# Kernel optimization log

Hardware: AMD Instinct MI355X
Metric: run time of the kernel (lower is better)

Reference implementation:

```python
import jax, jax.numpy as jnp
import numpy as np

B, K, D = 4, 4096, 2048

def setup_inputs() -> dict:
    key = jax.random.key(0)
    k1, k2, k3 = jax.random.split(key, 3)
    x = jax.random.normal(k1, (B, K, D), dtype=jnp.float32)
    # Conv1d(dim, dim, kernel_size=1) weight [D, D, 1] squeezed to a dense [D_out, D_in] matrix
    W = jax.random.normal(k2, (D, D), dtype=jnp.float32) / np.sqrt(D)
    b = jax.random.normal(k3, (D,), dtype=jnp.float32) * 0.02
    return {"x": x, "W": W, "b": b}

def reference(x, W, b):
    # lam_t = sigmoid(dt_proj(u_t)); pointwise conv1d == per-timestep linear
    lam = jax.nn.sigmoid(jnp.einsum("bkd,ed->bke", x, W) + b)  # [B,K,D]
    # Gated linear recurrence: s_t = lam_t * s_{t-1} + (1 - lam_t) * u_t
    def step(s, inp):
        lam_t, u_t = inp  # each [B,D]
        s = lam_t * s + (1.0 - lam_t) * u_t
        return s, s
    s0 = jnp.zeros((x.shape[0], x.shape[2]), dtype=x.dtype)
    _, ys = jax.lax.scan(step, s0, (jnp.moveaxis(lam, 1, 0), jnp.moveaxis(x, 1, 0)))
    return jnp.moveaxis(ys, 0, 1)  # [B,K,D]
```

## Files before the change

### kernel.cpp

```cpp
#include <hip/hip_runtime.h>
#include <hip/hip_bf16.h>

#define B_SZ 4
#define K_SEQ 4096
#define D_DIM 2048
#define M_ROWS (B_SZ * K_SEQ)

#define BM 128
#define BN 128
#define BK 32

#define CHUNK 64
#define NCHUNK (K_SEQ / CHUNK)

typedef __attribute__((ext_vector_type(8))) short short8;
typedef __attribute__((ext_vector_type(4))) float floatx4;
typedef __attribute__((ext_vector_type(8))) unsigned short ushortx8;

__device__ __forceinline__ unsigned short f2bf_rne(float f) {
  unsigned int u = __float_as_uint(f);
  u += 0x7fffu + ((u >> 16) & 1u);
  return (unsigned short)(u >> 16);
}
__device__ __forceinline__ float bf2f(unsigned short u) {
  return __uint_as_float(((unsigned int)u) << 16);
}

#define NX4 (M_ROWS * D_DIM / 4)
#define NW4 (D_DIM * D_DIM / 4)
__global__ void cvt_bf16_kernel(const float* __restrict__ x,
                                const float* __restrict__ W,
                                unsigned short* __restrict__ xb,
                                unsigned short* __restrict__ Wb) {
  int i = blockIdx.x * blockDim.x + threadIdx.x;
  const float* src;
  unsigned short* dst;
  int j;
  if (i < NX4) { src = x; dst = xb; j = i; }
  else         { src = W; dst = Wb; j = i - NX4; }
  float4 v = ((const float4*)src)[j];
  ushort4 o;
  o.x = f2bf_rne(v.x);
  o.y = f2bf_rne(v.y);
  o.z = f2bf_rne(v.z);
  o.w = f2bf_rne(v.w);
  ((ushort4*)dst)[j] = o;
}

__device__ __forceinline__ void gl_lds16(const void* g, void* l) {
  __builtin_amdgcn_global_load_lds(
      (const __attribute__((address_space(1))) unsigned int*)g,
      (__attribute__((address_space(3))) unsigned int*)l, 16, 0, 0);
}

template <bool GBF>
__global__ __launch_bounds__(256)
void gemm_lam_kernel(const unsigned short* __restrict__ A,
                     const unsigned short* __restrict__ Wb,
                     const float* __restrict__ bias,
                     void* __restrict__ lamv) {
  __shared__ __align__(16) unsigned short As[BM * BK];
  __shared__ __align__(16) unsigned short Bs[BN * BK];

  const int tid = threadIdx.x;
  const int lane = tid & 63;
  const int wave = tid >> 6;
  const int bm = blockIdx.x * BM;
  const int bn = blockIdx.y * BN;
  const int wr = (wave >> 1) * 64;
  const int wc = (wave & 1) * 64;
  const int lrow = lane & 15;
  const int kgrp = lane >> 4;

  floatx4 acc[4][4];
#pragma unroll
  for (int i = 0; i < 4; ++i)
#pragma unroll
    for (int j = 0; j < 4; ++j)
      acc[i][j] = (floatx4){0.f, 0.f, 0.f, 0.f};

  const int c0 = tid, c1 = tid + 256;
  const int r0 = c0 >> 2, q0 = (c0 & 3) ^ ((r0 >> 1) & 3);
  const int r1 = c1 >> 2, q1 = (c1 & 3) ^ ((r1 >> 1) & 3);
  const unsigned short* gA0 = A + (size_t)(bm + r0) * D_DIM + (q0 << 3);
  const unsigned short* gA1 = A + (size_t)(bm + r1) * D_DIM + (q1 << 3);
  const unsigned short* gB0 = Wb + (size_t)(bn + r0) * D_DIM + (q0 << 3);
  const unsigned short* gB1 = Wb + (size_t)(bn + r1) * D_DIM + (q1 << 3);
  unsigned short* lA0 = As + c0 * 8;
  unsigned short* lA1 = As + c1 * 8;
  unsigned short* lB0 = Bs + c0 * 8;
  unsigned short* lB1 = Bs + c1 * 8;

  const int kq_s = kgrp ^ ((lrow >> 1) & 3);

  for (int k0 = 0; k0 < D_DIM; k0 += BK) {
    gl_lds16(gA0 + k0, lA0);
    gl_lds16(gA1 + k0, lA1);
    gl_lds16(gB0 + k0, lB0);
    gl_lds16(gB1 + k0, lB1);
    __syncthreads();

    short8 af[4], bf[4];
#pragma unroll
    for (int i = 0; i < 4; ++i) {
      const int rowA = wr + i * 16 + lrow;
      const int rowB = wc + i * 16 + lrow;
      af[i] = *(const short8*)(As + rowA * 32 + kq_s * 8);
      bf[i] = *(const short8*)(Bs + rowB * 32 + kq_s * 8);
    }
#pragma unroll
    for (int mi = 0; mi < 4; ++mi)
#pragma unroll
      for (int ni = 0; ni < 4; ++ni)
        acc[mi][ni] = __builtin_amdgcn_mfma_f32_16x16x32_bf16(
            af[mi], bf[ni], acc[mi][ni], 0, 0, 0);
    __syncthreads();
  }

  const int crow = (lane >> 4) << 2;
  const int ccol = lane & 15;
#pragma unroll
  for (int ni = 0; ni < 4; ++ni) {
    const int ge = bn + wc + ni * 16 + ccol;
    const float bb = bias[ge];
#pragma unroll
    for (int mi = 0; mi < 4; ++mi) {
      const int gm0 = bm + wr + mi * 16 + crow;
#pragma unroll
      for (int r = 0; r < 4; ++r) {
        float v = acc[mi][ni][r] + bb;
        size_t off = (size_t)(gm0 + r) * D_DIM + ge;
        if constexpr (GBF) {
          float g = 1.0f / (1.0f + __expf(v));
          ((unsigned short*)lamv)[off] = f2bf_rne(g);
        } else {
          ((float*)lamv)[off] = 1.0f / (1.0f + __expf(-v));
        }
      }
    }
  }
}


__global__ void scan_reduce_bf(const unsigned short* __restrict__ gb,
                               const unsigned short* __restrict__ xb,
                               float* __restrict__ Ach,
                               float* __restrict__ Bch) {
  int idx = blockIdx.x * blockDim.x + threadIdx.x;
  int d8 = idx & 255;
  int c = (idx >> 8) & (NCHUNK - 1);
  int b = idx >> 14;
  size_t base = ((size_t)(b * K_SEQ + c * CHUNK)) * D_DIM + d8 * 8;
  float A[8], Bv[8];
#pragma unroll
  for (int j = 0; j < 8; ++j) { A[j] = 1.f; Bv[j] = 0.f; }
#pragma unroll 8
  for (int t = 0; t < CHUNK; ++t) {
    size_t o = base + (size_t)t * D_DIM;
    ushortx8 g8 = *(const ushortx8*)(gb + o);
    ushortx8 u8 = *(const ushortx8*)(xb + o);
#pragma unroll
    for (int j = 0; j < 8; ++j) {
      float g = bf2f(g8[j]), u = bf2f(u8[j]);
      A[j] -= g * A[j];
      Bv[j] += g * (u - Bv[j]);
    }
  }
  float4 a0 = make_float4(A[0], A[1], A[2], A[3]);
  float4 a1 = make_float4(A[4], A[5], A[6], A[7]);
  float4 b0 = make_float4(Bv[0], Bv[1], Bv[2], Bv[3]);
  float4 b1 = make_float4(Bv[4], Bv[5], Bv[6], Bv[7]);
  ((float4*)Ach)[idx * 2] = a0;
  ((float4*)Ach)[idx * 2 + 1] = a1;
  ((float4*)Bch)[idx * 2] = b0;
  ((float4*)Bch)[idx * 2 + 1] = b1;
}

__global__ void scan_prefix_kernel(const float* __restrict__ Ach,
                                   const float* __restrict__ Bch,
                                   float* __restrict__ Sst) {
  int idx = blockIdx.x * blockDim.x + threadIdx.x;
  int d4 = idx & (D_DIM / 4 - 1);
  int b = idx >> 9;
  float4 s = make_float4(0.f, 0.f, 0.f, 0.f);
#pragma unroll 4
  for (int c = 0; c < NCHUNK; ++c) {
    int o4 = (b * NCHUNK + c) * (D_DIM / 4) + d4;
    ((float4*)Sst)[o4] = s;
    float4 A = ((const float4*)Ach)[o4];
    float4 Bv = ((const float4*)Bch)[o4];
    s.x = A.x * s.x + Bv.x;
    s.y = A.y * s.y + Bv.y;
    s.z = A.z * s.z + Bv.z;
    s.w = A.w * s.w + Bv.w;
  }
}

__global__ void scan_apply_bf(const unsigned short* __restrict__ gb,
                              const unsigned short* __restrict__ xb,
                              const float* __restrict__ Sst,
                              float* __restrict__ out) {
  int idx = blockIdx.x * blockDim.x + threadIdx.x;
  int d8 = idx & 255;
  int c = (idx >> 8) & (NCHUNK - 1);
  int b = idx >> 14;
  size_t base = ((size_t)(b * K_SEQ + c * CHUNK)) * D_DIM + d8 * 8;
  float4 s0 = ((const float4*)Sst)[idx * 2];
  float4 s1 = ((const float4*)Sst)[idx * 2 + 1];
  float s[8] = {s0.x, s0.y, s0.z, s0.w, s1.x, s1.y, s1.z, s1.w};
#pragma unroll 8
  for (int t = 0; t < CHUNK; ++t) {
    size_t o = base + (size_t)t * D_DIM;
    ushortx8 g8 = *(const ushortx8*)(gb + o);
    ushortx8 u8 = *(const ushortx8*)(xb + o);
#pragma unroll
    for (int j = 0; j < 8; ++j) {
      float g = bf2f(g8[j]), u = bf2f(u8[j]);
      s[j] += g * (u - s[j]);
    }
    *(float4*)(out + o) = make_float4(s[0], s[1], s[2], s[3]);
    *(float4*)(out + o + 4) = make_float4(s[4], s[5], s[6], s[7]);
  }
}

__global__ void scan_reduce_kernel(const float* __restrict__ lam,
                                   const unsigned short* __restrict__ xb,
                                   float* __restrict__ Ach,
                                   float* __restrict__ Bch) {
  int idx = blockIdx.x * blockDim.x + threadIdx.x;
  int d4 = idx & (D_DIM / 4 - 1);
  int c = (idx >> 9) & (NCHUNK - 1);
  int b = idx >> 15;
  size_t base = ((size_t)(b * K_SEQ + c * CHUNK)) * D_DIM + d4 * 4;
  float4 Aacc = make_float4(1.f, 1.f, 1.f, 1.f);
  float4 Bv = make_float4(0.f, 0.f, 0.f, 0.f);
#pragma unroll 4
  for (int t = 0; t < CHUNK; ++t) {
    size_t o = base + (size_t)t * D_DIM;
    float4 l = *(const float4*)(lam + o);
    ushort4 ub = *(const ushort4*)(xb + o);
    Aacc.x *= l.x; Bv.x = l.x * (Bv.x - bf2f(ub.x)) + bf2f(ub.x);
    Aacc.y *= l.y; Bv.y = l.y * (Bv.y - bf2f(ub.y)) + bf2f(ub.y);
    Aacc.z *= l.z; Bv.z = l.z * (Bv.z - bf2f(ub.z)) + bf2f(ub.z);
    Aacc.w *= l.w; Bv.w = l.w * (Bv.w - bf2f(ub.w)) + bf2f(ub.w);
  }
  ((float4*)Ach)[idx] = Aacc;
  ((float4*)Bch)[idx] = Bv;
}

__global__ void scan_apply_kernel(float* lamout,
                                  const unsigned short* __restrict__ xb,
                                  const float* __restrict__ Sst) {
  int idx = blockIdx.x * blockDim.x + threadIdx.x;
  int d4 = idx & (D_DIM / 4 - 1);
  int c = (idx >> 9) & (NCHUNK - 1);
  int b = idx >> 15;
  size_t base = ((size_t)(b * K_SEQ + c * CHUNK)) * D_DIM + d4 * 4;
  float4 s = ((const float4*)Sst)[idx];
#pragma unroll 4
  for (int t = 0; t < CHUNK; ++t) {
    size_t o = base + (size_t)t * D_DIM;
    float4 l = *(const float4*)(lamout + o);
    ushort4 ub = *(const ushort4*)(xb + o);
    s.x = l.x * (s.x - bf2f(ub.x)) + bf2f(ub.x);
    s.y = l.y * (s.y - bf2f(ub.y)) + bf2f(ub.y);
    s.z = l.z * (s.z - bf2f(ub.z)) + bf2f(ub.z);
    s.w = l.w * (s.w - bf2f(ub.w)) + bf2f(ub.w);
    *(float4*)(lamout + o) = s;
  }
}

extern "C" void kernel_launch(void* const* d_in, const int* in_sizes, int n_in,
                              void* d_out, int out_size, void* d_ws, size_t ws_size,
                              hipStream_t stream) {
  const float* x = (const float*)d_in[0];
  const float* W = (const float*)d_in[1];
  const float* bias = (const float*)d_in[2];
  float* out = (float*)d_out;

  char* ws = (char*)d_ws;
  const size_t NEED_BF = 148897792ULL;
  const bool bfpath = (ws_size >= NEED_BF);

  unsigned short* x_bf = (unsigned short*)ws;
  unsigned short* W_bf = (unsigned short*)(ws + 67108864ULL);

  cvt_bf16_kernel<<<(NX4 + NW4) / 256, 256, 0, stream>>>(x, W, x_bf, W_bf);

  if (bfpath) {
    unsigned short* g_bf = (unsigned short*)(ws + 75497472ULL);
    float* Ach = (float*)(ws + 142606336ULL);
    float* Bch = (float*)(ws + 144703488ULL);
    float* Sst = (float*)(ws + 146800640ULL);

    dim3 grid(M_ROWS / BM, D_DIM / BN);
    gemm_lam_kernel<true><<<grid, 256, 0, stream>>>(x_bf, W_bf, bias, g_bf);

    int total8 = B_SZ * NCHUNK * D_DIM / 8;
    scan_reduce_bf<<<total8 / 256, 256, 0, stream>>>(g_bf, x_bf, Ach, Bch);
    scan_prefix_kernel<<<(B_SZ * D_DIM / 4) / 256, 256, 0, stream>>>(Ach, Bch, Sst);
    scan_apply_bf<<<total8 / 256, 256, 0, stream>>>(g_bf, x_bf, Sst, out);
  } else {
    float* Ach = (float*)(ws + 75497472ULL);
    float* Bch = (float*)(ws + 77594624ULL);
    float* Sst = (float*)(ws + 79691776ULL);

    dim3 grid(M_ROWS / BM, D_DIM / BN);
    gemm_lam_kernel<false><<<grid, 256, 0, stream>>>(x_bf, W_bf, bias, out);

    int total4 = B_SZ * NCHUNK * D_DIM / 4;
    scan_reduce_kernel<<<total4 / 256, 256, 0, stream>>>(out, x_bf, Ach, Bch);
    scan_prefix_kernel<<<(B_SZ * D_DIM / 4) / 256, 256, 0, stream>>>(Ach, Bch, Sst);
    scan_apply_kernel<<<total4 / 256, 256, 0, stream>>>(out, x_bf, Sst);
  }
}
```

Before: 476.8 us.

## Replace GEMM with 256x256 multi-stage pipelined 8-wave kernel; narrow scan vectors

The lambda GEMM moves from 128x128 single-buffered tiles with 4 waves to 256x256 tiles with 8 waves. It uses a 4-slot LDS ring fed by global_load_lds with prefetch three stages ahead, plus explicit vmcnt/lgkmcnt waits, barriers and setprio around MFMA bursts. The aim is to hide global-memory latency and raise reuse per loaded byte. The scan reduce/apply kernels switch from 8 to 4 elements per thread, giving more threads and smaller per-thread loads. The larger LDS footprint (128KB) and register pressure limit occupancy, and the hand-placed waitcnts carry some correctness risk.

```diff
diff --git a/kernel.cpp b/kernel.cpp
--- a/kernel.cpp
+++ b/kernel.cpp
@@ -5,10 +5,6 @@
 #define K_SEQ 4096
 #define D_DIM 2048
 #define M_ROWS (B_SZ * K_SEQ)
-
-#define BM 128
-#define BN 128
-#define BK 32
 
 #define CHUNK 64
 #define NCHUNK (K_SEQ / CHUNK)
@@ -54,81 +50,118 @@
 }
 
 template <bool GBF>
-__global__ __launch_bounds__(256)
-void gemm_lam_kernel(const unsigned short* __restrict__ A,
-                     const unsigned short* __restrict__ Wb,
-                     const float* __restrict__ bias,
-                     void* __restrict__ lamv) {
-  __shared__ __align__(16) unsigned short As[BM * BK];
-  __shared__ __align__(16) unsigned short Bs[BN * BK];
+__global__ __launch_bounds__(512, 2)
+void gemm8_kernel(const unsigned short* __restrict__ Ag,
+                  const unsigned short* __restrict__ Wg,
+                  const float* __restrict__ bias,
+                  void* __restrict__ lamv) {
+  __shared__ __align__(16) unsigned short smem[65536];
 
   const int tid = threadIdx.x;
   const int lane = tid & 63;
   const int wave = tid >> 6;
-  const int bm = blockIdx.x * BM;
-  const int bn = blockIdx.y * BN;
-  const int wr = (wave >> 1) * 64;
-  const int wc = (wave & 1) * 64;
-  const int lrow = lane & 15;
-  const int kgrp = lane >> 4;
-
-  floatx4 acc[4][4];
-#pragma unroll
-  for (int i = 0; i < 4; ++i)
+  const int wr = wave >> 2;
+  const int wc = wave & 3;
+  const int bm = (blockIdx.x >> 3) * 256;
+  const int bn = (blockIdx.x & 7) * 256;
+
+  const int lane15 = lane & 15;
+  const int choff = (((lane >> 4) ^ (lane & 3)) << 3);
+  const int rA_off = (wr * 128 + lane15) * 32 + choff;
+  const int rB_off = (wc * 64 + lane15) * 32 + choff;
+
+  const int r_s = tid >> 2;
+  const int ch_l = (tid & 3) ^ (r_s & 3);
+  const unsigned short* gA0 = Ag + (size_t)(bm + r_s) * D_DIM + ch_l * 8;
+  const unsigned short* gA1 = gA0 + (size_t)128 * D_DIM;
+  const unsigned short* gB0 = Wg + (size_t)(bn + r_s) * D_DIM + ch_l * 8;
+  const unsigned short* gB1 = gB0 + (size_t)128 * D_DIM;
+  const int st_off = tid * 8;
+
+  floatx4 acc[8][4];
+#pragma unroll
+  for (int i = 0; i < 8; ++i)
 #pragma unroll
     for (int j = 0; j < 4; ++j)
       acc[i][j] = (floatx4){0.f, 0.f, 0.f, 0.f};
 
-  const int c0 = tid, c1 = tid + 256;
-  const int r0 = c0 >> 2, q0 = (c0 & 3) ^ ((r0 >> 1) & 3);
-  const int r1 = c1 >> 2, q1 = (c1 & 3) ^ ((r1 >> 1) & 3);
-  const unsigned short* gA0 = A + (size_t)(bm + r0) * D_DIM + (q0 << 3);
-  const unsigned short* gA1 = A + (size_t)(bm + r1) * D_DIM + (q1 << 3);
-  const unsigned short* gB0 = Wb + (size_t)(bn + r0) * D_DIM + (q0 << 3);
-  const unsigned short* gB1 = Wb + (size_t)(bn + r1) * D_DIM + (q1 << 3);
-  unsigned short* lA0 = As + c0 * 8;
-  unsigned short* lA1 = As + c1 * 8;
-  unsigned short* lB0 = Bs + c0 * 8;
-  unsigned short* lB1 = Bs + c1 * 8;
-
-  const int kq_s = kgrp ^ ((lrow >> 1) & 3);
-
-  for (int k0 = 0; k0 < D_DIM; k0 += BK) {
-    gl_lds16(gA0 + k0, lA0);
-    gl_lds16(gA1 + k0, lA1);
-    gl_lds16(gB0 + k0, lB0);
-    gl_lds16(gB1 + k0, lB1);
-    __syncthreads();
-
-    short8 af[4], bf[4];
-#pragma unroll
-    for (int i = 0; i < 4; ++i) {
-      const int rowA = wr + i * 16 + lrow;
-      const int rowB = wc + i * 16 + lrow;
-      af[i] = *(const short8*)(As + rowA * 32 + kq_s * 8);
-      bf[i] = *(const short8*)(Bs + rowB * 32 + kq_s * 8);
-    }
-#pragma unroll
-    for (int mi = 0; mi < 4; ++mi)
-#pragma unroll
-      for (int ni = 0; ni < 4; ++ni)
-        acc[mi][ni] = __builtin_amdgcn_mfma_f32_16x16x32_bf16(
-            af[mi], bf[ni], acc[mi][ni], 0, 0, 0);
-    __syncthreads();
-  }
+#pragma unroll
+  for (int jt = 0; jt < 3; ++jt) {
+    const int ts = jt * 16384;
+    gl_lds16(gA0 + jt * 32, smem + ts + st_off);
+    gl_lds16(gA1 + jt * 32, smem + ts + 4096 + st_off);
+    gl_lds16(gB0 + jt * 32, smem + ts + 8192 + st_off);
+    gl_lds16(gB1 + jt * 32, smem + ts + 12288 + st_off);
+  }
+  asm volatile("s_waitcnt vmcnt(8)" ::: "memory");
+  __builtin_amdgcn_s_barrier();
+
+#define PAIR(J, STG, VMA)                                                     \
+  {                                                                           \
+    const int slot = (J) & 3;                                                 \
+    const unsigned short* sA = smem + slot * 16384;                           \
+    const unsigned short* sB = sA + 8192;                                     \
+    short8 bfr[4], afr[4];                                                    \
+    _Pragma("unroll") for (int nf = 0; nf < 4; ++nf)                          \
+        bfr[nf] = *(const short8*)(sB + rB_off + nf * 512);                   \
+    _Pragma("unroll") for (int mf = 0; mf < 4; ++mf)                          \
+        afr[mf] = *(const short8*)(sA + rA_off + mf * 512);                   \
+    if (STG) {                                                                \
+      const int jt = (J) + 3;                                                 \
+      const int ts = (jt & 3) * 16384;                                        \
+      gl_lds16(gA0 + jt * 32, smem + ts + st_off);                            \
+      gl_lds16(gA1 + jt * 32, smem + ts + 4096 + st_off);                     \
+    }                                                                         \
+    __builtin_amdgcn_s_barrier();                                             \
+    asm volatile("s_waitcnt lgkmcnt(0)" ::: "memory");                        \
+    __builtin_amdgcn_s_setprio(1);                                            \
+    _Pragma("unroll") for (int mf = 0; mf < 4; ++mf)                          \
+      _Pragma("unroll") for (int nf = 0; nf < 4; ++nf)                        \
+        acc[mf][nf] = __builtin_amdgcn_mfma_f32_16x16x32_bf16(                \
+            afr[mf], bfr[nf], acc[mf][nf], 0, 0, 0);                          \
+    __builtin_amdgcn_s_setprio(0);                                            \
+    __builtin_amdgcn_s_barrier();                                             \
+    _Pragma("unroll") for (int mf = 0; mf < 4; ++mf)                          \
+        afr[mf] = *(const short8*)(sA + rA_off + 2048 + mf * 512);            \
+    if (STG) {                                                                \
+      const int jt = (J) + 3;                                                 \
+      const int ts = (jt & 3) * 16384 + 8192;                                 \
+      gl_lds16(gB0 + jt * 32, smem + ts + st_off);                            \
+      gl_lds16(gB1 + jt * 32, smem + ts + 4096 + st_off);                     \
+    }                                                                         \
+    if ((VMA) == 8) asm volatile("s_waitcnt vmcnt(8)" ::: "memory");          \
+    else if ((VMA) == 4) asm volatile("s_waitcnt vmcnt(4)" ::: "memory");     \
+    else if ((VMA) == 0) asm volatile("s_waitcnt vmcnt(0)" ::: "memory");     \
+    __builtin_amdgcn_s_barrier();                                             \
+    asm volatile("s_waitcnt lgkmcnt(0)" ::: "memory");                        \
+    __builtin_amdgcn_s_setprio(1);                                            \
+    _Pragma("unroll") for (int mf = 0; mf < 4; ++mf)                          \
+      _Pragma("unroll") for (int nf = 0; nf < 4; ++nf)                        \
+        acc[mf + 4][nf] = __builtin_amdgcn_mfma_f32_16x16x32_bf16(            \
+            afr[mf], bfr[nf], acc[mf + 4][nf], 0, 0, 0);                      \
+    __builtin_amdgcn_s_setprio(0);                                            \
+    __builtin_amdgcn_s_barrier();                                             \
+  }
+
+#pragma unroll 4
+  for (int j = 0; j < 60; ++j) PAIR(j, true, 8);
+  PAIR(60, true, 8);
+  PAIR(61, false, 4);
+  PAIR(62, false, 0);
+  PAIR(63, false, -1);
+#undef PAIR
 
   const int crow = (lane >> 4) << 2;
-  const int ccol = lane & 15;
-#pragma unroll
-  for (int ni = 0; ni < 4; ++ni) {
-    const int ge = bn + wc + ni * 16 + ccol;
+#pragma unroll
+  for (int nf = 0; nf < 4; ++nf) {
+    const int ge = bn + wc * 64 + nf * 16 + lane15;
     const float bb = bias[ge];
 #pragma unroll
-    for (int mi = 0; mi < 4; ++mi) {
-      const int gm0 = bm + wr + mi * 16 + crow;
+    for (int mf = 0; mf < 8; ++mf) {
+      const int gm0 = bm + wr * 128 + mf * 16 + crow;
 #pragma unroll
       for (int r = 0; r < 4; ++r) {
-        float v = acc[mi][ni][r] + bb;
+        float v = acc[mf][nf][r] + bb;
         size_t off = (size_t)(gm0 + r) * D_DIM + ge;
         if constexpr (GBF) {
           float g = 1.0f / (1.0f + __expf(v));
@@ -147,33 +180,26 @@
                                float* __restrict__ Ach,
                                float* __restrict__ Bch) {
   int idx = blockIdx.x * blockDim.x + threadIdx.x;
-  int d8 = idx & 255;
-  int c = (idx >> 8) & (NCHUNK - 1);
-  int b = idx >> 14;
-  size_t base = ((size_t)(b * K_SEQ + c * CHUNK)) * D_DIM + d8 * 8;
-  float A[8], Bv[8];
-#pragma unroll
-  for (int j = 0; j < 8; ++j) { A[j] = 1.f; Bv[j] = 0.f; }
+  int d4 = idx & 511;
+  int c = (idx >> 9) & (NCHUNK - 1);
+  int b = idx >> 15;
+  size_t base = ((size_t)(b * K_SEQ + c * CHUNK)) * D_DIM + d4 * 4;
+  float A[4], Bv[4];
+#pragma unroll
+  for (int j = 0; j < 4; ++j) { A[j] = 1.f; Bv[j] = 0.f; }
 #pragma unroll 8
   for (int t = 0; t < CHUNK; ++t) {
     size_t o = base + (size_t)t * D_DIM;
-    ushortx8 g8 = *(const ushortx8*)(gb + o);
-    ushortx8 u8 = *(const ushortx8*)(xb + o);
-#pragma unroll
-    for (int j = 0; j < 8; ++j) {
-      float g = bf2f(g8[j]), u = bf2f(u8[j]);
-      A[j] -= g * A[j];
-      Bv[j] += g * (u - Bv[j]);
-    }
-  }
-  float4 a0 = make_float4(A[0], A[1], A[2], A[3]);
-  float4 a1 = make_float4(A[4], A[5], A[6], A[7]);
-  float4 b0 = make_float4(Bv[0], Bv[1], Bv[2], Bv[3]);
-  float4 b1 = make_float4(Bv[4], Bv[5], Bv[6], Bv[7]);
-  ((float4*)Ach)[idx * 2] = a0;
-  ((float4*)Ach)[idx * 2 + 1] = a1;
-  ((float4*)Bch)[idx * 2] = b0;
-  ((float4*)Bch)[idx * 2 + 1] = b1;
+    ushort4 g4 = *(const ushort4*)(gb + o);
+    ushort4 u4 = *(const ushort4*)(xb + o);
+    float g, u;
+    g = bf2f(g4.x); u = bf2f(u4.x); A[0] -= g * A[0]; Bv[0] += g * (u - Bv[0]);
+    g = bf2f(g4.y); u = bf2f(u4.y); A[1] -= g * A[1]; Bv[1] += g * (u - Bv[1]);
+    g = bf2f(g4.z); u = bf2f(u4.z); A[2] -= g * A[2]; Bv[2] += g * (u - Bv[2]);
+    g = bf2f(g4.w); u = bf2f(u4.w); A[3] -= g * A[3]; Bv[3] += g * (u - Bv[3]);
+  }
+  ((float4*)Ach)[idx] = make_float4(A[0], A[1], A[2], A[3]);
+  ((float4*)Bch)[idx] = make_float4(Bv[0], Bv[1], Bv[2], Bv[3]);
 }
 
 __global__ void scan_prefix_kernel(const float* __restrict__ Ach,
@@ -201,25 +227,22 @@
                               const float* __restrict__ Sst,
                               float* __restrict__ out) {
   int idx = blockIdx.x * blockDim.x + threadIdx.x;
-  int d8 = idx & 255;
-  int c = (idx >> 8) & (NCHUNK - 1);
-  int b = idx >> 14;
-  size_t base = ((size_t)(b * K_SEQ + c * CHUNK)) * D_DIM + d8 * 8;
-  float4 s0 = ((const float4*)Sst)[idx * 2];
-  float4 s1 = ((const float4*)Sst)[idx * 2 + 1];
-  float s[8] = {s0.x, s0.y, s0.z, s0.w, s1.x, s1.y, s1.z, s1.w};
+  int d4 = idx & 511;
+  int c = (idx >> 9) & (NCHUNK - 1);
+  int b = idx >> 15;
+  size_t base = ((size_t)(b * K_SEQ + c * CHUNK)) * D_DIM + d4 * 4;
+  float4 s4 = ((const float4*)Sst)[idx];
+  float s[4] = {s4.x, s4.y, s4.z, s4.w};
 #pragma unroll 8
   for (int t = 0; t < CHUNK; ++t) {
     size_t o = base + (size_t)t * D_DIM;
-    ushortx8 g8 = *(const ushortx8*)(gb + o);
-    ushortx8 u8 = *(const ushortx8*)(xb + o);
-#pragma unroll
-    for (int j = 0; j < 8; ++j) {
-      float g = bf2f(g8[j]), u = bf2f(u8[j]);
-      s[j] += g * (u - s[j]);
-    }
+    ushort4 g4 = *(const ushort4*)(gb + o);
+    ushort4 u4 = *(const ushort4*)(xb + o);
+    s[0] += bf2f(g4.x) * (bf2f(u4.x) - s[0]);
+    s[1] += bf2f(g4.y) * (bf2f(u4.y) - s[1]);
+    s[2] += bf2f(g4.z) * (bf2f(u4.z) - s[2]);
+    s[3] += bf2f(g4.w) * (bf2f(u4.w) - s[3]);
     *(float4*)(out + o) = make_float4(s[0], s[1], s[2], s[3]);
-    *(float4*)(out + o + 4) = make_float4(s[4], s[5], s[6], s[7]);
   }
 }
 
@@ -287,26 +310,26 @@
 
   cvt_bf16_kernel<<<(NX4 + NW4) / 256, 256, 0, stream>>>(x, W, x_bf, W_bf);
 
+  dim3 ggrid((M_ROWS / 256) * (D_DIM / 256));
+
   if (bfpath) {
     unsigned short* g_bf = (unsigned short*)(ws + 75497472ULL);
     float* Ach = (float*)(ws + 142606336ULL);
     float* Bch = (float*)(ws + 144703488ULL);
     float* Sst = (float*)(ws + 146800640ULL);
 
-    dim3 grid(M_ROWS / BM, D_DIM / BN);
-    gemm_lam_kernel<true><<<grid, 256, 0, stream>>>(x_bf, W_bf, bias, g_bf);
-
-    int total8 = B_SZ * NCHUNK * D_DIM / 8;
-    scan_reduce_bf<<<total8 / 256, 256, 0, stream>>>(g_bf, x_bf, Ach, Bch);
+    gemm8_kernel<true><<<ggrid, 512, 0, stream>>>(x_bf, W_bf, bias, g_bf);
+
+    int total4 = B_SZ * NCHUNK * D_DIM / 4;
+    scan_reduce_bf<<<total4 / 256, 256, 0, stream>>>(g_bf, x_bf, Ach, Bch);
     scan_prefix_kernel<<<(B_SZ * D_DIM / 4) / 256, 256, 0, stream>>>(Ach, Bch, Sst);
-    scan_apply_bf<<<total8 / 256, 256, 0, stream>>>(g_bf, x_bf, Sst, out);
+    scan_apply_bf<<<total4 / 256, 256, 0, stream>>>(g_bf, x_bf, Sst, out);
   } else {
     float* Ach = (float*)(ws + 75497472ULL);
     float* Bch = (float*)(ws + 77594624ULL);
     float* Sst = (float*)(ws + 79691776ULL);
 
-    dim3 grid(M_ROWS / BM, D_DIM / BN);
-    gemm_lam_kernel<false><<<grid, 256, 0, stream>>>(x_bf, W_bf, bias, out);
+    gemm8_kernel<false><<<ggrid, 512, 0, stream>>>(x_bf, W_bf, bias, out);
 
     int total4 = B_SZ * NCHUNK * D_DIM / 4;
     scan_reduce_kernel<<<total4 / 256, 256, 0, stream>>>(out, x_bf, Ach, Bch);
```

After: 455.8 us. 1.05x faster.

## Replace GEMM with 256x256 double-buffered 8-wave kernel and halve scan chunk

Applied to the files above, without the earlier changes.

Replaces the 128x128 single-stage GEMM with a 512-thread, 256x256-tile kernel. It double-buffers K-tiles in 128KB of LDS using direct global-to-LDS loads, and interleaves staging, barriers, and MFMA phases with explicit vmcnt/lgkmcnt waits and setprio. The aim is to raise operand reuse per LDS byte and hide global-load latency behind MFMA work. Separately, the scan chunk size drops from 64 to 32 for more parallelism in the reduce and apply passes, at the cost of a longer prefix pass. Workspace offsets are rearranged so the chunk buffers reuse the W_bf region, which is safe only because W_bf is no longer needed after the GEMM.

```diff
diff --git a/kernel.cpp b/kernel.cpp
--- a/kernel.cpp
+++ b/kernel.cpp
@@ -6,11 +6,7 @@
 #define D_DIM 2048
 #define M_ROWS (B_SZ * K_SEQ)
 
-#define BM 128
-#define BN 128
-#define BK 32
-
-#define CHUNK 64
+#define CHUNK 32
 #define NCHUNK (K_SEQ / CHUNK)
 
 typedef __attribute__((ext_vector_type(8))) short short8;
@@ -53,82 +49,144 @@
       (__attribute__((address_space(3))) unsigned int*)l, 16, 0, 0);
 }
 
+#define WAITVM_(n) asm volatile("s_waitcnt vmcnt(" #n ")" ::: "memory")
+#define WAITVM(n) WAITVM_(n)
+
 template <bool GBF>
-__global__ __launch_bounds__(256)
-void gemm_lam_kernel(const unsigned short* __restrict__ A,
-                     const unsigned short* __restrict__ Wb,
-                     const float* __restrict__ bias,
-                     void* __restrict__ lamv) {
-  __shared__ __align__(16) unsigned short As[BM * BK];
-  __shared__ __align__(16) unsigned short Bs[BN * BK];
+__global__ __launch_bounds__(512, 2)
+void gemm8_kernel(const unsigned short* __restrict__ Ag,
+                  const unsigned short* __restrict__ Wg,
+                  const float* __restrict__ bias,
+                  void* __restrict__ lamv) {
+  __shared__ __align__(16) unsigned short smem[65536];
 
   const int tid = threadIdx.x;
   const int lane = tid & 63;
   const int wave = tid >> 6;
-  const int bm = blockIdx.x * BM;
-  const int bn = blockIdx.y * BN;
-  const int wr = (wave >> 1) * 64;
-  const int wc = (wave & 1) * 64;
-  const int lrow = lane & 15;
-  const int kgrp = lane >> 4;
-
-  floatx4 acc[4][4];
-#pragma unroll
-  for (int i = 0; i < 4; ++i)
+  const int wr = wave >> 2;
+  const int wc = wave & 3;
+  const int bm = (blockIdx.x >> 3) * 256;
+  const int bn = (blockIdx.x & 7) * 256;
+
+  const int lane15 = lane & 15;
+  const int tA = (wr == 0) ? 0 : 3;
+  const int tB = (wc < 2) ? 1 : 2;
+  const int sw16 = ((lane >> 2) & 1) << 4;
+  const int kg8 = (lane >> 4) << 3;
+  const int rA15 = lane15 * 64 + (kg8 ^ sw16);
+  const int bb15 = ((wc & 1) << 12) + rA15;
+
+  const int r_s = tid >> 3;
+  const int lcol = (((tid & 7) ^ (((tid >> 5) & 1) << 1)) << 3);
+  const unsigned short* gA0p = Ag + (size_t)(bm + r_s) * D_DIM + lcol;
+  const unsigned short* gA1p = Ag + (size_t)(bm + 128 + r_s) * D_DIM + lcol;
+  const unsigned short* gB0p = Wg + (size_t)(bn + r_s) * D_DIM + lcol;
+  const unsigned short* gB1p = Wg + (size_t)(bn + 128 + r_s) * D_DIM + lcol;
+  const int st8 = tid * 8;
+
+#define STG(T, gp, jt)                                                        \
+  {                                                                           \
+    unsigned short* d_ = smem + (((T) + (((jt) & 1) << 2)) << 13) + st8;      \
+    const unsigned short* s_ = (gp) + ((size_t)(jt) << 6);                    \
+    gl_lds16(s_, d_);                                                         \
+    gl_lds16(s_ + 64 * (size_t)D_DIM, d_ + 4096);                             \
+  }
+
+  floatx4 acc[8][4];
+#pragma unroll
+  for (int i = 0; i < 8; ++i)
 #pragma unroll
     for (int j = 0; j < 4; ++j)
       acc[i][j] = (floatx4){0.f, 0.f, 0.f, 0.f};
 
-  const int c0 = tid, c1 = tid + 256;
-  const int r0 = c0 >> 2, q0 = (c0 & 3) ^ ((r0 >> 1) & 3);
-  const int r1 = c1 >> 2, q1 = (c1 & 3) ^ ((r1 >> 1) & 3);
-  const unsigned short* gA0 = A + (size_t)(bm + r0) * D_DIM + (q0 << 3);
-  const unsigned short* gA1 = A + (size_t)(bm + r1) * D_DIM + (q1 << 3);
-  const unsigned short* gB0 = Wb + (size_t)(bn + r0) * D_DIM + (q0 << 3);
-  const unsigned short* gB1 = Wb + (size_t)(bn + r1) * D_DIM + (q1 << 3);
-  unsigned short* lA0 = As + c0 * 8;
-  unsigned short* lA1 = As + c1 * 8;
-  unsigned short* lB0 = Bs + c0 * 8;
-  unsigned short* lB1 = Bs + c1 * 8;
-
-  const int kq_s = kgrp ^ ((lrow >> 1) & 3);
-
-  for (int k0 = 0; k0 < D_DIM; k0 += BK) {
-    gl_lds16(gA0 + k0, lA0);
-    gl_lds16(gA1 + k0, lA1);
-    gl_lds16(gB0 + k0, lB0);
-    gl_lds16(gB1 + k0, lB1);
-    __syncthreads();
-
-    short8 af[4], bf[4];
-#pragma unroll
-    for (int i = 0; i < 4; ++i) {
-      const int rowA = wr + i * 16 + lrow;
-      const int rowB = wc + i * 16 + lrow;
-      af[i] = *(const short8*)(As + rowA * 32 + kq_s * 8);
-      bf[i] = *(const short8*)(Bs + rowB * 32 + kq_s * 8);
-    }
-#pragma unroll
-    for (int mi = 0; mi < 4; ++mi)
-#pragma unroll
-      for (int ni = 0; ni < 4; ++ni)
-        acc[mi][ni] = __builtin_amdgcn_mfma_f32_16x16x32_bf16(
-            af[mi], bf[ni], acc[mi][ni], 0, 0, 0);
-    __syncthreads();
-  }
+#define MFMA16(AB, AF, BF)                                                    \
+  _Pragma("unroll") for (int mf = 0; mf < 4; ++mf)                            \
+  _Pragma("unroll") for (int nf = 0; nf < 4; ++nf)                            \
+      acc[(AB) + mf][nf] = __builtin_amdgcn_mfma_f32_16x16x32_bf16(           \
+          AF[mf], BF[nf], acc[(AB) + mf][nf], 0, 0, 0);
+
+  STG(0, gA0p, 0);
+  STG(1, gB0p, 0);
+  STG(3, gA1p, 0);
+  STG(2, gB1p, 0);
+  STG(0, gA0p, 1);
+  WAITVM(2);
+  __builtin_amdgcn_s_barrier();
+
+#define TILE(j, DOS1, DOS2, DOS4, V4)                                         \
+  {                                                                           \
+    const unsigned short* pA =                                                \
+        smem + ((tA + (((j) & 1) << 2)) << 13) + rA15;                        \
+    const unsigned short* pB =                                                \
+        smem + ((tB + (((j) & 1) << 2)) << 13) + bb15;                        \
+    short8 a0k0[4], a0k1[4], a1k0[4], a1k1[4], bk0[4], bk1[4];                \
+                         \
+    _Pragma("unroll") for (int mf = 0; mf < 4; ++mf) {                        \
+      a0k0[mf] = *(const short8*)(pA + mf * 1024);                            \
+      a0k1[mf] = *(const short8*)(pA + mf * 1024 + 32);                       \
+    }                                                                         \
+    _Pragma("unroll") for (int nf = 0; nf < 4; ++nf)                          \
+        bk0[nf] = *(const short8*)(pB + nf * 1024);                           \
+    if (DOS1) { STG(1, gB0p, (j) + 1); STG(3, gA1p, (j) + 1); }               \
+    __builtin_amdgcn_s_barrier();                                             \
+    asm volatile("s_waitcnt lgkmcnt(0)" ::: "memory");                        \
+    __builtin_amdgcn_sched_barrier(0);                                        \
+    __builtin_amdgcn_s_setprio(1);                                            \
+    MFMA16(0, a0k0, bk0);                                                     \
+    __builtin_amdgcn_s_setprio(0);                                            \
+                                 \
+    _Pragma("unroll") for (int mf = 0; mf < 4; ++mf) {                        \
+      a1k0[mf] = *(const short8*)(pA + 4096 + mf * 1024);                     \
+      a1k1[mf] = *(const short8*)(pA + 4096 + mf * 1024 + 32);                \
+    }                                                                         \
+    if (DOS2) { STG(2, gB1p, (j) + 1); }                                      \
+    __builtin_amdgcn_s_barrier();                                             \
+    asm volatile("s_waitcnt lgkmcnt(0)" ::: "memory");                        \
+    __builtin_amdgcn_sched_barrier(0);                                        \
+    __builtin_amdgcn_s_setprio(1);                                            \
+    MFMA16(4, a1k0, bk0);                                                     \
+    __builtin_amdgcn_s_setprio(0);                                            \
+                                              \
+    _Pragma("unroll") for (int nf = 0; nf < 4; ++nf)                          \
+        bk1[nf] = *(const short8*)(pB + nf * 1024 + 32);                      \
+    __builtin_amdgcn_s_barrier();                                             \
+    asm volatile("s_waitcnt lgkmcnt(0)" ::: "memory");                        \
+    __builtin_amdgcn_sched_barrier(0);                                        \
+    __builtin_amdgcn_s_setprio(1);                                            \
+    MFMA16(4, a1k1, bk1);                                                     \
+    __builtin_amdgcn_s_setprio(0);                                            \
+          \
+          \
+    if (DOS4) { STG(0, gA0p, (j) + 2); }                                      \
+    if ((V4) == 2) { WAITVM(2); }                                             \
+    else if ((V4) == 0) { WAITVM(0); }                                        \
+    __builtin_amdgcn_s_barrier();                                             \
+    asm volatile("s_waitcnt lgkmcnt(0)" ::: "memory");                        \
+    __builtin_amdgcn_sched_barrier(0);                                        \
+    __builtin_amdgcn_s_setprio(1);                                            \
+    MFMA16(0, a0k1, bk1);                                                     \
+    __builtin_amdgcn_s_setprio(0);                                            \
+  }
+
+#pragma unroll 2
+  for (int j = 0; j < 30; ++j) TILE(j, 1, 1, 1, 2);
+  TILE(30, 1, 1, 0, 0);
+  TILE(31, 0, 0, 0, -1);
+#undef TILE
+#undef STG
+#undef MFMA16
 
   const int crow = (lane >> 4) << 2;
-  const int ccol = lane & 15;
-#pragma unroll
-  for (int ni = 0; ni < 4; ++ni) {
-    const int ge = bn + wc + ni * 16 + ccol;
+#pragma unroll
+  for (int nf = 0; nf < 4; ++nf) {
+    const int ge = bn + wc * 64 + nf * 16 + lane15;
     const float bb = bias[ge];
 #pragma unroll
-    for (int mi = 0; mi < 4; ++mi) {
-      const int gm0 = bm + wr + mi * 16 + crow;
+    for (int mf = 0; mf < 8; ++mf) {
+      const int gm0 = bm + wr * 128 + mf * 16 + crow;
 #pragma unroll
       for (int r = 0; r < 4; ++r) {
-        float v = acc[mi][ni][r] + bb;
+        float v = acc[mf][nf][r] + bb;
         size_t off = (size_t)(gm0 + r) * D_DIM + ge;
         if constexpr (GBF) {
           float g = 1.0f / (1.0f + __expf(v));
@@ -149,7 +207,7 @@
   int idx = blockIdx.x * blockDim.x + threadIdx.x;
   int d8 = idx & 255;
   int c = (idx >> 8) & (NCHUNK - 1);
-  int b = idx >> 14;
+  int b = idx >> 15;
   size_t base = ((size_t)(b * K_SEQ + c * CHUNK)) * D_DIM + d8 * 8;
   float A[8], Bv[8];
 #pragma unroll
@@ -203,7 +261,7 @@
   int idx = blockIdx.x * blockDim.x + threadIdx.x;
   int d8 = idx & 255;
   int c = (idx >> 8) & (NCHUNK - 1);
-  int b = idx >> 14;
+  int b = idx >> 15;
   size_t base = ((size_t)(b * K_SEQ + c * CHUNK)) * D_DIM + d8 * 8;
   float4 s0 = ((const float4*)Sst)[idx * 2];
   float4 s1 = ((const float4*)Sst)[idx * 2 + 1];
@@ -230,7 +288,7 @@
   int idx = blockIdx.x * blockDim.x + threadIdx.x;
   int d4 = idx & (D_DIM / 4 - 1);
   int c = (idx >> 9) & (NCHUNK - 1);
-  int b = idx >> 15;
+  int b = idx >> 16;
   size_t base = ((size_t)(b * K_SEQ + c * CHUNK)) * D_DIM + d4 * 4;
   float4 Aacc = make_float4(1.f, 1.f, 1.f, 1.f);
   float4 Bv = make_float4(0.f, 0.f, 0.f, 0.f);
@@ -254,7 +312,7 @@
   int idx = blockIdx.x * blockDim.x + threadIdx.x;
   int d4 = idx & (D_DIM / 4 - 1);
   int c = (idx >> 9) & (NCHUNK - 1);
-  int b = idx >> 15;
+  int b = idx >> 16;
   size_t base = ((size_t)(b * K_SEQ + c * CHUNK)) * D_DIM + d4 * 4;
   float4 s = ((const float4*)Sst)[idx];
 #pragma unroll 4
@@ -287,14 +345,15 @@
 
   cvt_bf16_kernel<<<(NX4 + NW4) / 256, 256, 0, stream>>>(x, W, x_bf, W_bf);
 
+  dim3 ggrid((M_ROWS / 256) * (D_DIM / 256));
+
   if (bfpath) {
     unsigned short* g_bf = (unsigned short*)(ws + 75497472ULL);
-    float* Ach = (float*)(ws + 142606336ULL);
-    float* Bch = (float*)(ws + 144703488ULL);
-    float* Sst = (float*)(ws + 146800640ULL);
-
-    dim3 grid(M_ROWS / BM, D_DIM / BN);
-    gemm_lam_kernel<true><<<grid, 256, 0, stream>>>(x_bf, W_bf, bias, g_bf);
+    float* Ach = (float*)(ws + 67108864ULL);
+    float* Bch = (float*)(ws + 71303168ULL);
+    float* Sst = (float*)(ws + 142606336ULL);
+
+    gemm8_kernel<true><<<ggrid, 512, 0, stream>>>(x_bf, W_bf, bias, g_bf);
 
     int total8 = B_SZ * NCHUNK * D_DIM / 8;
     scan_reduce_bf<<<total8 / 256, 256, 0, stream>>>(g_bf, x_bf, Ach, Bch);
@@ -302,11 +361,10 @@
     scan_apply_bf<<<total8 / 256, 256, 0, stream>>>(g_bf, x_bf, Sst, out);
   } else {
     float* Ach = (float*)(ws + 75497472ULL);
-    float* Bch = (float*)(ws + 77594624ULL);
-    float* Sst = (float*)(ws + 79691776ULL);
-
-    dim3 grid(M_ROWS / BM, D_DIM / BN);
-    gemm_lam_kernel<false><<<grid, 256, 0, stream>>>(x_bf, W_bf, bias, out);
+    float* Bch = (float*)(ws + 79691776ULL);
+    float* Sst = (float*)(ws + 83886080ULL);
+
+    gemm8_kernel<false><<<ggrid, 512, 0, stream>>>(x_bf, W_bf, bias, out);
 
     int total4 = B_SZ * NCHUNK * D_DIM / 4;
     scan_reduce_kernel<<<total4 / 256, 256, 0, stream>>>(out, x_bf, Ach, Bch);
```

Measured after the change: 439.6 us. -7.8%, faster.
